# Kernel tuning notes

Hardware: AMD Instinct MI355X
Metric: run time of the kernel (lower is better)

## Reference

```python
import jax, jax.numpy as jnp
import numpy as np

DIM = 192
HEADS = 6
HEAD_DIM = DIM // HEADS
WH, WW = 8, 8
N = WH * WW
SCALE = HEAD_DIM ** -0.5


def relative_position_index(wh, ww):
    ch, cw = np.meshgrid(np.arange(wh), np.arange(ww), indexing='ij')
    coords = np.stack([ch.ravel(), cw.ravel()])            # [2, N]
    rel = coords[:, :, None] - coords[:, None, :]          # [2, N, N]
    rel = rel.transpose(1, 2, 0)
    rel[:, :, 0] += wh - 1
    rel[:, :, 1] += ww - 1
    rel[:, :, 0] *= 2 * ww - 1
    return jnp.asarray(rel.sum(-1))                        # [N, N] int


REL_IDX = relative_position_index(WH, WW)


def setup_inputs() -> dict:
    key = jax.random.key(0)
    ks = jax.random.split(key, 12)
    B_ = 4096
    nW = 64
    s = DIM ** -0.5
    inp = {
        'lr_up_windows': jax.random.normal(ks[0], (B_, N, DIM), jnp.float32),
        'ref_down_up_windows': jax.random.normal(ks[1], (B_, N, DIM), jnp.float32),
        'ref_windows': jax.random.normal(ks[2], (B_, N, DIM), jnp.float32),
        'mask': jnp.zeros((nW, N, N), jnp.float32),
        'Wq': jax.random.normal(ks[3], (DIM, DIM), jnp.float32) * s,
        'bq': jnp.zeros((DIM,), jnp.float32),
        'Wk': jax.random.normal(ks[4], (DIM, DIM), jnp.float32) * s,
        'bk': jnp.zeros((DIM,), jnp.float32),
        'Wv': jax.random.normal(ks[5], (DIM, DIM), jnp.float32) * s,
        'bv': jnp.zeros((DIM,), jnp.float32),
        'Wp': jax.random.normal(ks[6], (DIM, DIM), jnp.float32) * s,
        'bp': jnp.zeros((DIM,), jnp.float32),
        'bias_table': jax.random.normal(ks[7], ((2 * WH - 1) * (2 * WW - 1), HEADS), jnp.float32) * 0.02,
    }
    return inp


def reference(lr_up_windows, ref_down_up_windows, ref_windows, mask,
              Wq, bq, Wk, bk, Wv, bv, Wp, bp, bias_table):
    B_, n, C = lr_up_windows.shape
    # projections ([in, out] weights; x @ W + b)
    q = (lr_up_windows @ Wq + bq).reshape(B_, n, HEADS, HEAD_DIM).transpose(0, 2, 1, 3)
    k = (ref_down_up_windows @ Wk + bk).reshape(B_, n, HEADS, HEAD_DIM).transpose(0, 2, 1, 3)
    v = (ref_windows @ Wv + bv).reshape(B_, n, HEADS, HEAD_DIM).transpose(0, 2, 1, 3)
    attn = jnp.einsum('bhnd,bhmd->bhnm', q * SCALE, k)     # [B_, H, N, N]
    rpb = bias_table[REL_IDX]                               # [N, N, H]
    attn = attn + rpb.transpose(2, 0, 1)[None]
    nW = mask.shape[0]
    attn = attn.reshape(B_ // nW, nW, HEADS, n, n) + mask[None, :, None]
    attn = attn.reshape(B_, HEADS, n, n)
    attn = jax.nn.softmax(attn, axis=-1)
    x = jnp.einsum('bhnm,bhmd->bhnd', attn, v).transpose(0, 2, 1, 3).reshape(B_, n, C)
    return x @ Wp + bp
```

## Files before the change

### kernel.cpp

```cpp
#include <hip/hip_runtime.h>
#include <hip/hip_bf16.h>
#include <stdint.h>

typedef short s16x8 __attribute__((ext_vector_type(8)));
typedef short s16x4 __attribute__((ext_vector_type(4)));
typedef float f32x4 __attribute__((ext_vector_type(4)));

#define MFMA16(a, b, c) __builtin_amdgcn_mfma_f32_16x16x32_bf16((a), (b), (c), 0, 0, 0)

__device__ __forceinline__ unsigned short f2bf(float f) {
  union { float f; uint32_t u; } x; x.f = f;
  uint32_t u = x.u;
  return (unsigned short)((u + 0x7FFFu + ((u >> 16) & 1u)) >> 16);
}
__device__ __forceinline__ float bf2f(unsigned short h) {
  union { uint32_t u; float f; } x; x.u = ((uint32_t)h) << 16;
  return x.f;
}
__device__ __forceinline__ void glds16(const void* g, void* l) {
  __builtin_amdgcn_global_load_lds((const __attribute__((address_space(1))) void*)g,
                                   (__attribute__((address_space(3))) void*)l, 16, 0, 0);
}

__global__ __launch_bounds__(256) void prep_weights(
    const float* __restrict__ Wq, const float* __restrict__ Wk,
    const float* __restrict__ Wv, const float* __restrict__ Wp,
    unsigned short* __restrict__ wt) {
  int idx = blockIdx.x * 256 + threadIdx.x;
  if (idx >= 4 * 36864) return;
  int mat = idx / 36864, rem = idx % 36864;
  int n = rem / 192, k = rem % 192;
  const float* W = (mat == 0) ? Wq : (mat == 1) ? Wk : (mat == 2) ? Wv : Wp;
  wt[idx] = f2bf(W[k * 192 + n]);
}

__global__ __launch_bounds__(256) void prep_rpb(
    const float* __restrict__ bias_table, unsigned short* __restrict__ rpb) {
  int idx = blockIdx.x * 256 + threadIdx.x;
  if (idx >= 6 * 4096) return;
  int h = idx / 4096, r = idx % 4096;
  int i = r >> 6, j = r & 63;
  int dh = (i >> 3) - (j >> 3) + 7;
  int dw = (i & 7) - (j & 7) + 7;
  rpb[idx] = f2bf(bias_table[(dh * 15 + dw) * 6 + h]);
}

__global__ __launch_bounds__(256, 2) void pass1_proj(
    const float* __restrict__ X1g, const float* __restrict__ X2g,
    const float* __restrict__ X3g,
    const float* __restrict__ bq, const float* __restrict__ bk,
    const float* __restrict__ bv,
    const unsigned short* __restrict__ wt,
    char* __restrict__ qkv, int B_) {
  extern __shared__ char p1lds[];
  float* xs = (float*)p1lds;
  char* ob = p1lds + 50176;
  const int which = blockIdx.x / B_;
  const int w = blockIdx.x - which * B_;
  const int tid = threadIdx.x;
  const int wv = tid >> 6, lane = tid & 63;
  const int l16 = lane & 15, lq = lane >> 4;
  const float* Xb =
      ((which == 0) ? X1g : (which == 1) ? X2g : X3g) + (size_t)w * 12288;
  const unsigned short* W = wt + which * 36864;
  const int nt0 = wv * 3;

#pragma unroll
  for (int rnd = 0; rnd < 13; ++rnd) {
    int cid = rnd * 256 + tid;
    if (rnd < 12 || tid < 64) {
      int row = cid / 49, c = cid - row * 49;
      int c2 = (c < 48) ? c : 47;
      glds16(Xb + row * 192 + c2 * 4, p1lds + (rnd * 256 + wv * 64) * 16);
    }
  }

  s16x8 wf[3][6];
#pragma unroll
  for (int t = 0; t < 3; ++t) {
    const unsigned short* wc = W + (size_t)((nt0 + t) * 16 + l16) * 192 + lq * 8;
#pragma unroll
    for (int ks = 0; ks < 6; ++ks) wf[t][ks] = *(const s16x8*)(wc + ks * 32);
  }
  f32x4 bqk[3];
  float bvv[3];
  if (which < 2) {
    const float* bias = which ? bk : bq;
#pragma unroll
    for (int t = 0; t < 3; ++t)
      bqk[t] = *(const f32x4*)&bias[(nt0 + t) * 16 + lq * 4];
  } else {
#pragma unroll
    for (int t = 0; t < 3; ++t) bvv[t] = bv[(nt0 + t) * 16 + l16];
  }
  __syncthreads();

  const float scale = (which == 0) ? 0.17677669529663689f : 1.0f;

#pragma unroll
  for (int mi = 0; mi < 4; ++mi) {
    s16x8 xf[6];
    const float* pr = xs + (mi * 16 + l16) * 196 + lq * 8;
#pragma unroll
    for (int ks = 0; ks < 6; ++ks) {
      float4 v0 = *(const float4*)(pr + ks * 32);
      float4 v1 = *(const float4*)(pr + ks * 32 + 4);
      s16x8 t;
      t[0] = (short)f2bf(v0.x); t[1] = (short)f2bf(v0.y);
      t[2] = (short)f2bf(v0.z); t[3] = (short)f2bf(v0.w);
      t[4] = (short)f2bf(v1.x); t[5] = (short)f2bf(v1.y);
      t[6] = (short)f2bf(v1.z); t[7] = (short)f2bf(v1.w);
      xf[ks] = t;
    }
    if (which < 2) {
      int tok = mi * 16 + l16;
#pragma unroll
      for (int t = 0; t < 3; ++t) {
        f32x4 acc = bqk[t];
#pragma unroll
        for (int ks = 0; ks < 6; ++ks) acc = MFMA16(wf[t][ks], xf[ks], acc);
        s16x4 pv;
#pragma unroll
        for (int q = 0; q < 4; ++q) pv[q] = (short)f2bf(acc[q] * scale);
        int c = (nt0 + t) * 2 + (lq >> 1);
        *(s16x4*)(ob + tok * 384 + ((c ^ (tok & 7)) << 4) + (lq & 1) * 8) = pv;
      }
    } else {
#pragma unroll
      for (int t = 0; t < 3; ++t) {
        f32x4 acc = {bvv[t], bvv[t], bvv[t], bvv[t]};
#pragma unroll
        for (int ks = 0; ks < 6; ++ks) acc = MFMA16(xf[ks], wf[t][ks], acc);
        int d = (nt0 + t) * 16 + l16;
        int c = (mi >> 1) * 4 + lq;
        s16x4 pv;
#pragma unroll
        for (int q = 0; q < 4; ++q) pv[q] = (short)f2bf(acc[q]);
        *(s16x4*)(ob + d * 128 + ((c ^ (d & 7)) << 4) + (mi & 1) * 8) = pv;
      }
    }
  }
  __syncthreads();

  char* gdst = qkv + (size_t)w * 73728 + which * 24576;
#pragma unroll
  for (int r = 0; r < 6; ++r) {
    int i = (r * 256 + tid) * 16;
    *(float4*)(gdst + i) = *(const float4*)(ob + i);
  }
}

__global__ __launch_bounds__(512, 4) void pass2_attn(
    const char* __restrict__ qkv, const float* __restrict__ maskg,
    const unsigned short* __restrict__ rpb, const float* __restrict__ bp,
    const unsigned short* __restrict__ wt, float* __restrict__ out, int nW) {
  extern __shared__ char lds[];
  const int b = blockIdx.x, tid = threadIdx.x;
  const int wv = tid >> 6, lane = tid & 63;
  const int l16 = lane & 15, lq = lane >> 4;
  const char* Qg = qkv + (size_t)b * 73728;
  const char* KVsrc = Qg + 24576;

#pragma unroll
  for (int r = 0; r < 6; ++r)
    glds16(KVsrc + (size_t)(r * 512 + tid) * 16, lds + (r * 512 + wv * 64) * 16);

  const int mt = wv & 3, g = wv >> 2;
  const int row0 = mt * 16, qg = row0 + l16;
  s16x8 qf[3];
#pragma unroll
  for (int hh = 0; hh < 3; ++hh) {
    int c = (g * 3 + hh) * 4 + lq;
    qf[hh] = *(const s16x8*)(Qg + qg * 384 + ((c ^ (qg & 7)) << 4));
  }
  const float* mrow = maskg + (size_t)(b % nW) * 4096 + qg * 64;
  f32x4 mv[4];
#pragma unroll
  for (int nt = 0; nt < 4; ++nt) mv[nt] = *(const f32x4*)(mrow + nt * 16 + lq * 4);
  s16x4 rv[3][4];
#pragma unroll
  for (int hh = 0; hh < 3; ++hh)
#pragma unroll
    for (int nt = 0; nt < 4; ++nt)
      rv[hh][nt] = *(const s16x4*)&rpb[(g * 3 + hh) * 4096 + qg * 64 + nt * 16 + lq * 4];
  __syncthreads();

  unsigned short* Osm = (unsigned short*)(lds + 49152);
#pragma unroll
  for (int hh = 0; hh < 3; ++hh) {
    int h = g * 3 + hh;
    f32x4 sv[4];
#pragma unroll
    for (int nt = 0; nt < 4; ++nt) {
      int kr = nt * 16 + l16;
      s16x8 ka = *(const s16x8*)(lds + kr * 384 + (((h * 4 + lq) ^ (kr & 7)) << 4));
      f32x4 z = {0.f, 0.f, 0.f, 0.f};
      sv[nt] = MFMA16(ka, qf[hh], z);
    }
    float lg[4][4];
#pragma unroll
    for (int nt = 0; nt < 4; ++nt)
#pragma unroll
      for (int qr = 0; qr < 4; ++qr)
        lg[nt][qr] = sv[nt][qr] + bf2f((unsigned short)rv[hh][nt][qr]) + mv[nt][qr];
    float mx = lg[0][0];
#pragma unroll
    for (int nt = 0; nt < 4; ++nt)
#pragma unroll
      for (int qr = 0; qr < 4; ++qr) mx = fmaxf(mx, lg[nt][qr]);
    mx = fmaxf(mx, __shfl_xor(mx, 16, 64));
    mx = fmaxf(mx, __shfl_xor(mx, 32, 64));
    float p[4][4], sum = 0.f;
#pragma unroll
    for (int nt = 0; nt < 4; ++nt)
#pragma unroll
      for (int qr = 0; qr < 4; ++qr) {
        p[nt][qr] = __expf(lg[nt][qr] - mx);
        sum += p[nt][qr];
      }
    sum += __shfl_xor(sum, 16, 64);
    sum += __shfl_xor(sum, 32, 64);
    float ri = 1.0f / sum;
    s16x8 pa0, pa1;
#pragma unroll
    for (int r = 0; r < 4; ++r) {
      pa0[r]     = (short)f2bf(p[0][r] * ri);
      pa0[4 + r] = (short)f2bf(p[1][r] * ri);
      pa1[r]     = (short)f2bf(p[2][r] * ri);
      pa1[4 + r] = (short)f2bf(p[3][r] * ri);
    }
    f32x4 o0 = {0.f, 0.f, 0.f, 0.f};
    f32x4 o1 = {0.f, 0.f, 0.f, 0.f};
#pragma unroll
    for (int kt = 0; kt < 2; ++kt) {
      int d0 = h * 32 + l16, d1 = h * 32 + 16 + l16;
      s16x8 vb0 = *(const s16x8*)(lds + 24576 + d0 * 128 +
                                  ((((kt << 2) + lq) ^ (d0 & 7)) << 4));
      s16x8 vb1 = *(const s16x8*)(lds + 24576 + d1 * 128 +
                                  ((((kt << 2) + lq) ^ (d1 & 7)) << 4));
      o0 = MFMA16(kt ? pa1 : pa0, vb0, o0);
      o1 = MFMA16(kt ? pa1 : pa0, vb1, o1);
    }
#pragma unroll
    for (int q = 0; q < 4; ++q) {
      int row = row0 + lq * 4 + q;
      Osm[row * 208 + h * 32 + l16]      = f2bf(o0[q]);
      Osm[row * 208 + h * 32 + 16 + l16] = f2bf(o1[q]);
    }
  }
  __syncthreads();

  {
    const unsigned short* W = wt + 3 * 36864;
    float* obp = out + (size_t)b * 12288;
    const int mh = wv >> 2, nh = wv & 3;
    s16x8 a[2][6];
#pragma unroll
    for (int mi = 0; mi < 2; ++mi)
#pragma unroll
      for (int ks = 0; ks < 6; ++ks)
        a[mi][ks] = *(const s16x8*)&Osm[((mh * 2 + mi) * 16 + l16) * 208 +
                                        ks * 32 + lq * 8];
#pragma unroll
    for (int nt2 = 0; nt2 < 3; ++nt2) {
      int col = (nh * 3 + nt2) * 16 + l16;
      float bsv = bp[col];
      f32x4 acc0 = {bsv, bsv, bsv, bsv};
      f32x4 acc1 = {bsv, bsv, bsv, bsv};
      const unsigned short* wc = W + (size_t)col * 192 + lq * 8;
#pragma unroll
      for (int ks = 0; ks < 6; ++ks) {
        s16x8 bb = *(const s16x8*)(wc + ks * 32);
        acc0 = MFMA16(a[0][ks], bb, acc0);
        acc1 = MFMA16(a[1][ks], bb, acc1);
      }
#pragma unroll
      for (int q = 0; q < 4; ++q) {
        obp[((mh * 2 + 0) * 16 + lq * 4 + q) * 192 + col] = acc0[q];
        obp[((mh * 2 + 1) * 16 + lq * 4 + q) * 192 + col] = acc1[q];
      }
    }
  }
}

#define XPAD 200
#define VPAD 72
#define PPAD 72
#define MPAD 66
struct SmemF {
  unsigned short Xs[2][64][XPAD];
  unsigned short Qs[64][XPAD];
  unsigned short Ks[64][XPAD];
  unsigned short VTs[192][VPAD];
  unsigned short Ps[2][64][PPAD];
  unsigned short Ms[64][MPAD];
};

__global__ __launch_bounds__(512, 2) void win_attn_fused(
    const float* __restrict__ X1g, const float* __restrict__ X2g,
    const float* __restrict__ X3g, const float* __restrict__ maskg,
    const float* __restrict__ bq, const float* __restrict__ bk,
    const float* __restrict__ bv, const float* __restrict__ bp,
    const unsigned short* __restrict__ wt, const unsigned short* __restrict__ rpb,
    float* __restrict__ out, int nW) {
  extern __shared__ char smem_raw[];
  SmemF& S = *reinterpret_cast<SmemF*>(smem_raw);
  const int b = blockIdx.x;
  const int tid = threadIdx.x;
  const int wave = tid >> 6, lane = tid & 63;
  const int l16 = lane & 15, lq = lane >> 4;
  const int mh = wave >> 2, nh = wave & 3;

  const float4* x1v = (const float4*)(X1g + (size_t)b * 12288);
  const float4* x2v = (const float4*)(X2g + (size_t)b * 12288);
  const float4* x3v = (const float4*)(X3g + (size_t)b * 12288);
  float4 x3r[6];
#pragma unroll
  for (int it = 0; it < 6; ++it) {
    int i = it * 512 + tid;
    float4 v1 = x1v[i];
    float4 v2 = x2v[i];
    x3r[it] = x3v[i];
    int row = i / 48, c = (i % 48) * 4;
    s16x4 p1, p2;
    p1[0] = (short)f2bf(v1.x); p1[1] = (short)f2bf(v1.y);
    p1[2] = (short)f2bf(v1.z); p1[3] = (short)f2bf(v1.w);
    p2[0] = (short)f2bf(v2.x); p2[1] = (short)f2bf(v2.y);
    p2[2] = (short)f2bf(v2.z); p2[3] = (short)f2bf(v2.w);
    *(s16x4*)&S.Xs[0][row][c] = p1;
    *(s16x4*)&S.Xs[1][row][c] = p2;
  }
  const float* mw = maskg + (size_t)(b % nW) * 4096;
  for (int i = tid; i < 4096; i += 512)
    S.Ms[i >> 6][i & 63] = f2bf(mw[i]);
  __syncthreads();

  auto proj = [&](const unsigned short (*Xsrc)[XPAD], const unsigned short* W,
                  const float* bias, unsigned short (*dst)[XPAD], float scale) {
    s16x8 a[2][6];
#pragma unroll
    for (int mi = 0; mi < 2; ++mi)
#pragma unroll
      for (int ks = 0; ks < 6; ++ks)
        a[mi][ks] = *(const s16x8*)&Xsrc[(mh * 2 + mi) * 16 + l16][ks * 32 + lq * 8];
#pragma unroll
    for (int nt2 = 0; nt2 < 3; ++nt2) {
      int col = (nh * 3 + nt2) * 16 + l16;
      float bsv = bias[col];
      f32x4 acc0 = {bsv, bsv, bsv, bsv};
      f32x4 acc1 = {bsv, bsv, bsv, bsv};
#pragma unroll
      for (int ks = 0; ks < 6; ++ks) {
        s16x8 bb = *(const s16x8*)&W[(size_t)col * 192 + ks * 32 + lq * 8];
        acc0 = MFMA16(a[0][ks], bb, acc0);
        acc1 = MFMA16(a[1][ks], bb, acc1);
      }
#pragma unroll
      for (int q = 0; q < 4; ++q) {
        dst[(mh * 2 + 0) * 16 + lq * 4 + q][col] = f2bf(acc0[q] * scale);
        dst[(mh * 2 + 1) * 16 + lq * 4 + q][col] = f2bf(acc1[q] * scale);
      }
    }
  };

  proj(S.Xs[0], wt + 0 * 36864, bq, S.Qs, 0.17677669529663689f);
  proj(S.Xs[1], wt + 1 * 36864, bk, S.Ks, 1.0f);
  __syncthreads();

#pragma unroll
  for (int it = 0; it < 6; ++it) {
    int i = it * 512 + tid;
    int row = i / 48, c = (i % 48) * 4;
    s16x4 p3;
    p3[0] = (short)f2bf(x3r[it].x); p3[1] = (short)f2bf(x3r[it].y);
    p3[2] = (short)f2bf(x3r[it].z); p3[3] = (short)f2bf(x3r[it].w);
    *(s16x4*)&S.Xs[0][row][c] = p3;
  }
  __syncthreads();

  {
    const unsigned short* W = wt + 2 * 36864;
    s16x8 a[2][6];
#pragma unroll
    for (int mi = 0; mi < 2; ++mi)
#pragma unroll
      for (int ks = 0; ks < 6; ++ks)
        a[mi][ks] = *(const s16x8*)&S.Xs[0][(mh * 2 + mi) * 16 + l16][ks * 32 + lq * 8];
#pragma unroll
    for (int nt2 = 0; nt2 < 3; ++nt2) {
      int col = (nh * 3 + nt2) * 16 + l16;
      float bsv = bv[col];
      f32x4 acc0 = {bsv, bsv, bsv, bsv};
      f32x4 acc1 = {bsv, bsv, bsv, bsv};
#pragma unroll
      for (int ks = 0; ks < 6; ++ks) {
        s16x8 bb = *(const s16x8*)&W[(size_t)col * 192 + ks * 32 + lq * 8];
        acc0 = MFMA16(a[0][ks], bb, acc0);
        acc1 = MFMA16(a[1][ks], bb, acc1);
      }
      s16x4 pv0, pv1;
#pragma unroll
      for (int q = 0; q < 4; ++q) { pv0[q] = (short)f2bf(acc0[q]); pv1[q] = (short)f2bf(acc1[q]); }
      *(s16x4*)&S.VTs[col][(mh * 2 + 0) * 16 + lq * 4] = pv0;
      *(s16x4*)&S.VTs[col][(mh * 2 + 1) * 16 + lq * 4] = pv1;
    }
  }
  __syncthreads();

  {
    const int mt = wave & 3, g = wave >> 2;
    const int row0 = mt * 16;
#pragma unroll 1
    for (int hh = 0; hh < 3; ++hh) {
      int h = g * 3 + hh;
      s16x8 qa = *(const s16x8*)&S.Qs[row0 + l16][h * 32 + lq * 8];
      f32x4 sv[4];
#pragma unroll
      for (int nt = 0; nt < 4; ++nt) {
        s16x8 kb = *(const s16x8*)&S.Ks[nt * 16 + l16][h * 32 + lq * 8];
        f32x4 z = {0.f, 0.f, 0.f, 0.f};
        sv[nt] = MFMA16(qa, kb, z);
      }
      const unsigned short* rpbh = rpb + h * 4096;
      float lg[4][4];
#pragma unroll
      for (int nt = 0; nt < 4; ++nt) {
        int j = nt * 16 + l16;
#pragma unroll
        for (int q = 0; q < 4; ++q) {
          int i = row0 + lq * 4 + q;
          lg[nt][q] = sv[nt][q] + bf2f(rpbh[i * 64 + j]) + bf2f(S.Ms[i][j]);
        }
      }
#pragma unroll
      for (int q = 0; q < 4; ++q) {
        float m = fmaxf(fmaxf(lg[0][q], lg[1][q]), fmaxf(lg[2][q], lg[3][q]));
#pragma unroll
        for (int s = 1; s < 16; s <<= 1) m = fmaxf(m, __shfl_xor(m, s, 64));
        float p[4], sum = 0.f;
#pragma unroll
        for (int nt = 0; nt < 4; ++nt) { p[nt] = __expf(lg[nt][q] - m); sum += p[nt]; }
#pragma unroll
        for (int s = 1; s < 16; s <<= 1) sum += __shfl_xor(sum, s, 64);
        float r = 1.0f / sum;
#pragma unroll
        for (int nt = 0; nt < 4; ++nt)
          S.Ps[g][row0 + lq * 4 + q][nt * 16 + l16] = f2bf(p[nt] * r);
      }
      f32x4 oacc[2] = {{0.f, 0.f, 0.f, 0.f}, {0.f, 0.f, 0.f, 0.f}};
#pragma unroll
      for (int kt = 0; kt < 2; ++kt) {
        s16x8 pa = *(const s16x8*)&S.Ps[g][row0 + l16][kt * 32 + lq * 8];
#pragma unroll
        for (int n2 = 0; n2 < 2; ++n2) {
          s16x8 vb = *(const s16x8*)&S.VTs[h * 32 + n2 * 16 + l16][kt * 32 + lq * 8];
          oacc[n2] = MFMA16(pa, vb, oacc[n2]);
        }
      }
#pragma unroll
      for (int n2 = 0; n2 < 2; ++n2)
#pragma unroll
        for (int q = 0; q < 4; ++q)
          S.Xs[1][row0 + lq * 4 + q][h * 32 + n2 * 16 + l16] = f2bf(oacc[n2][q]);
    }
  }
  __syncthreads();

  {
    const unsigned short* W = wt + 3 * 36864;
    float* ob = out + (size_t)b * 12288;
    s16x8 a[2][6];
#pragma unroll
    for (int mi = 0; mi < 2; ++mi)
#pragma unroll
      for (int ks = 0; ks < 6; ++ks)
        a[mi][ks] = *(const s16x8*)&S.Xs[1][(mh * 2 + mi) * 16 + l16][ks * 32 + lq * 8];
#pragma unroll
    for (int nt2 = 0; nt2 < 3; ++nt2) {
      int col = (nh * 3 + nt2) * 16 + l16;
      float bsv = bp[col];
      f32x4 acc0 = {bsv, bsv, bsv, bsv};
      f32x4 acc1 = {bsv, bsv, bsv, bsv};
#pragma unroll
      for (int ks = 0; ks < 6; ++ks) {
        s16x8 bb = *(const s16x8*)&W[(size_t)col * 192 + ks * 32 + lq * 8];
        acc0 = MFMA16(a[0][ks], bb, acc0);
        acc1 = MFMA16(a[1][ks], bb, acc1);
      }
#pragma unroll
      for (int q = 0; q < 4; ++q) {
        ob[((mh * 2 + 0) * 16 + lq * 4 + q) * 192 + col] = acc0[q];
        ob[((mh * 2 + 1) * 16 + lq * 4 + q) * 192 + col] = acc1[q];
      }
    }
  }
}

extern "C" void kernel_launch(void* const* d_in, const int* in_sizes, int n_in,
                              void* d_out, int out_size, void* d_ws, size_t ws_size,
                              hipStream_t stream) {
  const float* X1 = (const float*)d_in[0];
  const float* X2 = (const float*)d_in[1];
  const float* X3 = (const float*)d_in[2];
  const float* mask = (const float*)d_in[3];
  const float* Wq = (const float*)d_in[4];
  const float* bq = (const float*)d_in[5];
  const float* Wk = (const float*)d_in[6];
  const float* bk = (const float*)d_in[7];
  const float* Wv = (const float*)d_in[8];
  const float* bv = (const float*)d_in[9];
  const float* Wp = (const float*)d_in[10];
  const float* bp = (const float*)d_in[11];
  const float* bt = (const float*)d_in[12];

  unsigned short* wt = (unsigned short*)d_ws;
  unsigned short* rpb = wt + 4 * 36864;

  int B_ = in_sizes[0] / 12288;
  int nW = in_sizes[3] / 4096;

  prep_weights<<<576, 256, 0, stream>>>(Wq, Wk, Wv, Wp, wt);
  prep_rpb<<<96, 256, 0, stream>>>(bt, rpb);

  const size_t qkv_off = 344064;
  const size_t need = qkv_off + (size_t)B_ * 73728;

  if (ws_size >= need) {
    char* qkv = (char*)d_ws + qkv_off;
    (void)hipFuncSetAttribute((const void*)pass1_proj,
                              hipFuncAttributeMaxDynamicSharedMemorySize, 74752);
    pass1_proj<<<3 * B_, 256, 74752, stream>>>(X1, X2, X3, bq, bk, bv, wt, qkv, B_);
    (void)hipFuncSetAttribute((const void*)pass2_attn,
                              hipFuncAttributeMaxDynamicSharedMemorySize, 75776);
    pass2_attn<<<B_, 512, 75776, stream>>>(qkv, mask, rpb, bp, wt,
                                           (float*)d_out, nW);
  } else {
    (void)hipFuncSetAttribute((const void*)win_attn_fused,
                              hipFuncAttributeMaxDynamicSharedMemorySize,
                              (int)sizeof(SmemF));
    win_attn_fused<<<B_, 512, sizeof(SmemF), stream>>>(
        X1, X2, X3, mask, bq, bk, bv, bp, wt, rpb, (float*)d_out, nW);
  }
}
```

Measured before the change: 391.9 us.

## Shrink LDS in projection and attention passes to raise occupancy

Pass 1 now loads X through registers, converts it to bf16 once, and stores bf16 in LDS instead of fp32 staged by global_load_lds. This halves the input tile and removes the repeated per-row conversion. Pass 2 keeps softmax probabilities for all three heads in registers, adds a barrier, and writes attention output into the dead K region instead of a separate Osm buffer, cutting LDS to 48KB. Launch bounds are raised (3 and 6 blocks) to exploit the smaller footprint, at the cost of more register pressure and an extra barrier.

```diff
diff --git a/kernel.cpp b/kernel.cpp
--- a/kernel.cpp
+++ b/kernel.cpp
@@ -45,7 +45,7 @@
   rpb[idx] = f2bf(bias_table[(dh * 15 + dw) * 6 + h]);
 }
 
-__global__ __launch_bounds__(256, 2) void pass1_proj(
+__global__ __launch_bounds__(256, 3) void pass1_proj(
     const float* __restrict__ X1g, const float* __restrict__ X2g,
     const float* __restrict__ X3g,
     const float* __restrict__ bq, const float* __restrict__ bk,
@@ -53,26 +53,26 @@
     const unsigned short* __restrict__ wt,
     char* __restrict__ qkv, int B_) {
   extern __shared__ char p1lds[];
-  float* xs = (float*)p1lds;
-  char* ob = p1lds + 50176;
+  unsigned short* xs = (unsigned short*)p1lds;
+  char* ob = p1lds + 25600;
   const int which = blockIdx.x / B_;
   const int w = blockIdx.x - which * B_;
   const int tid = threadIdx.x;
-  const int wv = tid >> 6, lane = tid & 63;
+  const int lane = tid & 63;
+  const int wv = tid >> 6;
   const int l16 = lane & 15, lq = lane >> 4;
   const float* Xb =
       ((which == 0) ? X1g : (which == 1) ? X2g : X3g) + (size_t)w * 12288;
   const unsigned short* W = wt + which * 36864;
   const int nt0 = wv * 3;
 
-#pragma unroll
-  for (int rnd = 0; rnd < 13; ++rnd) {
-    int cid = rnd * 256 + tid;
-    if (rnd < 12 || tid < 64) {
-      int row = cid / 49, c = cid - row * 49;
-      int c2 = (c < 48) ? c : 47;
-      glds16(Xb + row * 192 + c2 * 4, p1lds + (rnd * 256 + wv * 64) * 16);
-    }
+  const float4* Xb4 = (const float4*)Xb;
+  float4 xr[12];
+#pragma unroll
+  for (int r = 0; r < 6; ++r) {
+    int p = r * 256 + tid;
+    xr[2 * r]     = Xb4[2 * p];
+    xr[2 * r + 1] = Xb4[2 * p + 1];
   }
 
   s16x8 wf[3][6];
@@ -93,6 +93,20 @@
 #pragma unroll
     for (int t = 0; t < 3; ++t) bvv[t] = bv[(nt0 + t) * 16 + l16];
   }
+
+#pragma unroll
+  for (int r = 0; r < 6; ++r) {
+    int p = r * 256 + tid;
+    int row = p / 24, k8 = p - row * 24;
+    const float4& a = xr[2 * r];
+    const float4& c = xr[2 * r + 1];
+    s16x8 t;
+    t[0] = (short)f2bf(a.x); t[1] = (short)f2bf(a.y);
+    t[2] = (short)f2bf(a.z); t[3] = (short)f2bf(a.w);
+    t[4] = (short)f2bf(c.x); t[5] = (short)f2bf(c.y);
+    t[6] = (short)f2bf(c.z); t[7] = (short)f2bf(c.w);
+    *(s16x8*)&xs[row * 200 + k8 * 8] = t;
+  }
   __syncthreads();
 
   const float scale = (which == 0) ? 0.17677669529663689f : 1.0f;
@@ -100,18 +114,9 @@
 #pragma unroll
   for (int mi = 0; mi < 4; ++mi) {
     s16x8 xf[6];
-    const float* pr = xs + (mi * 16 + l16) * 196 + lq * 8;
-#pragma unroll
-    for (int ks = 0; ks < 6; ++ks) {
-      float4 v0 = *(const float4*)(pr + ks * 32);
-      float4 v1 = *(const float4*)(pr + ks * 32 + 4);
-      s16x8 t;
-      t[0] = (short)f2bf(v0.x); t[1] = (short)f2bf(v0.y);
-      t[2] = (short)f2bf(v0.z); t[3] = (short)f2bf(v0.w);
-      t[4] = (short)f2bf(v1.x); t[5] = (short)f2bf(v1.y);
-      t[6] = (short)f2bf(v1.z); t[7] = (short)f2bf(v1.w);
-      xf[ks] = t;
-    }
+    const unsigned short* pr = xs + (mi * 16 + l16) * 200 + lq * 8;
+#pragma unroll
+    for (int ks = 0; ks < 6; ++ks) xf[ks] = *(const s16x8*)(pr + ks * 32);
     if (which < 2) {
       int tok = mi * 16 + l16;
 #pragma unroll
@@ -150,7 +155,7 @@
   }
 }
 
-__global__ __launch_bounds__(512, 4) void pass2_attn(
+__global__ __launch_bounds__(512, 6) void pass2_attn(
     const char* __restrict__ qkv, const float* __restrict__ maskg,
     const unsigned short* __restrict__ rpb, const float* __restrict__ bp,
     const unsigned short* __restrict__ wt, float* __restrict__ out, int nW) {
@@ -185,7 +190,7 @@
       rv[hh][nt] = *(const s16x4*)&rpb[(g * 3 + hh) * 4096 + qg * 64 + nt * 16 + lq * 4];
   __syncthreads();
 
-  unsigned short* Osm = (unsigned short*)(lds + 49152);
+  s16x8 pa[3][2];
 #pragma unroll
   for (int hh = 0; hh < 3; ++hh) {
     int h = g * 3 + hh;
@@ -221,14 +226,19 @@
     sum += __shfl_xor(sum, 16, 64);
     sum += __shfl_xor(sum, 32, 64);
     float ri = 1.0f / sum;
-    s16x8 pa0, pa1;
 #pragma unroll
     for (int r = 0; r < 4; ++r) {
-      pa0[r]     = (short)f2bf(p[0][r] * ri);
-      pa0[4 + r] = (short)f2bf(p[1][r] * ri);
-      pa1[r]     = (short)f2bf(p[2][r] * ri);
-      pa1[4 + r] = (short)f2bf(p[3][r] * ri);
-    }
+      pa[hh][0][r]     = (short)f2bf(p[0][r] * ri);
+      pa[hh][0][4 + r] = (short)f2bf(p[1][r] * ri);
+      pa[hh][1][r]     = (short)f2bf(p[2][r] * ri);
+      pa[hh][1][4 + r] = (short)f2bf(p[3][r] * ri);
+    }
+  }
+  __syncthreads();
+
+#pragma unroll
+  for (int hh = 0; hh < 3; ++hh) {
+    int h = g * 3 + hh;
     f32x4 o0 = {0.f, 0.f, 0.f, 0.f};
     f32x4 o1 = {0.f, 0.f, 0.f, 0.f};
 #pragma unroll
@@ -238,14 +248,18 @@
                                   ((((kt << 2) + lq) ^ (d0 & 7)) << 4));
       s16x8 vb1 = *(const s16x8*)(lds + 24576 + d1 * 128 +
                                   ((((kt << 2) + lq) ^ (d1 & 7)) << 4));
-      o0 = MFMA16(kt ? pa1 : pa0, vb0, o0);
-      o1 = MFMA16(kt ? pa1 : pa0, vb1, o1);
+      o0 = MFMA16(pa[hh][kt], vb0, o0);
+      o1 = MFMA16(pa[hh][kt], vb1, o1);
     }
 #pragma unroll
     for (int q = 0; q < 4; ++q) {
       int row = row0 + lq * 4 + q;
-      Osm[row * 208 + h * 32 + l16]      = f2bf(o0[q]);
-      Osm[row * 208 + h * 32 + 16 + l16] = f2bf(o1[q]);
+      int c0 = h * 4 + (l16 >> 3);
+      int c1 = c0 + 2;
+      *(unsigned short*)(lds + row * 384 + ((c0 ^ (row & 7)) << 4) +
+                         (l16 & 7) * 2) = f2bf(o0[q]);
+      *(unsigned short*)(lds + row * 384 + ((c1 ^ (row & 7)) << 4) +
+                         (l16 & 7) * 2) = f2bf(o1[q]);
     }
   }
   __syncthreads();
@@ -256,11 +270,13 @@
     const int mh = wv >> 2, nh = wv & 3;
     s16x8 a[2][6];
 #pragma unroll
-    for (int mi = 0; mi < 2; ++mi)
+    for (int mi = 0; mi < 2; ++mi) {
+      int row = (mh * 2 + mi) * 16 + l16;
 #pragma unroll
       for (int ks = 0; ks < 6; ++ks)
-        a[mi][ks] = *(const s16x8*)&Osm[((mh * 2 + mi) * 16 + l16) * 208 +
-                                        ks * 32 + lq * 8];
+        a[mi][ks] = *(const s16x8*)(lds + row * 384 +
+                                    ((((ks << 2) + lq) ^ (row & 7)) << 4));
+    }
 #pragma unroll
     for (int nt2 = 0; nt2 < 3; ++nt2) {
       int col = (nh * 3 + nt2) * 16 + l16;
@@ -528,11 +544,11 @@
   if (ws_size >= need) {
     char* qkv = (char*)d_ws + qkv_off;
     (void)hipFuncSetAttribute((const void*)pass1_proj,
-                              hipFuncAttributeMaxDynamicSharedMemorySize, 74752);
-    pass1_proj<<<3 * B_, 256, 74752, stream>>>(X1, X2, X3, bq, bk, bv, wt, qkv, B_);
+                              hipFuncAttributeMaxDynamicSharedMemorySize, 50176);
+    pass1_proj<<<3 * B_, 256, 50176, stream>>>(X1, X2, X3, bq, bk, bv, wt, qkv, B_);
     (void)hipFuncSetAttribute((const void*)pass2_attn,
-                              hipFuncAttributeMaxDynamicSharedMemorySize, 75776);
-    pass2_attn<<<B_, 512, 75776, stream>>>(qkv, mask, rpb, bp, wt,
+                              hipFuncAttributeMaxDynamicSharedMemorySize, 49152);
+    pass2_attn<<<B_, 512, 49152, stream>>>(qkv, mask, rpb, bp, wt,
                                            (float*)d_out, nW);
   } else {
     (void)hipFuncSetAttribute((const void*)win_attn_fused,
```

After: 419.5 us. 1.07x slower.
